# Kernel tuning notes

Hardware: AMD Instinct MI355X
Metric: run time of the kernel (lower is better)

The kernel has to match this reference:

```python
import jax, jax.numpy as jnp
import numpy as np

# --- constants matching DILConfig ---
N_DIFF = 1000      # num_diffusion_steps
STEPS = 4          # inference_steps
S_MAX = 4          # max_scales
BUDGET = 0.2       # entropy_budget
G0 = 2.0           # guidance_strength
ENT_LO = 0.1       # stability_threshold_low
ENT_HI = 0.5       # stability_threshold_high
B, L, C, H = 16, 1024, 128, 512


def setup_inputs() -> dict:
    key = jax.random.key(0)
    ks = jax.random.split(key, 6)
    y_obs = jax.random.normal(ks[0], (B, L, C), dtype=jnp.float32)
    mask = (jax.random.uniform(ks[1], (B, L, C)) > 0.5).astype(jnp.float32)
    z_init = jax.random.normal(ks[2], (B, L, C), dtype=jnp.float32)
    W1 = jax.random.normal(ks[3], (C, H), dtype=jnp.float32) / np.sqrt(C)
    b1 = jnp.zeros((H,), dtype=jnp.float32)
    W2 = jax.random.normal(ks[4], (H, C), dtype=jnp.float32) / np.sqrt(H)
    b2 = jnp.zeros((C,), dtype=jnp.float32)
    tw = jax.random.normal(ks[5], (H,), dtype=jnp.float32)
    return {"y_obs": y_obs, "mask": mask, "z_init": z_init,
            "W1": W1, "b1": b1, "W2": W2, "b2": b2, "tw": tw}


def _dil_forward(y_obs, mask, z_init, W1, b1, W2, b2, tw):
    # diffusion schedule (linear betas)
    betas = jnp.linspace(1e-4, 0.02, N_DIFF, dtype=jnp.float32)
    ac = jnp.cumprod(1.0 - betas)
    alpha = jnp.sqrt(ac)                     # sqrt_alphas_cumprod
    sigma = jnp.sqrt(1.0 - ac)               # sqrt_one_minus_alphas_cumprod
    lam = jnp.log(alpha) - jnp.log(sigma)    # log-SNR/2

    step = N_DIFF // STEPS
    ks = [N_DIFF - 1 - i * step for i in range(STEPS)]

    def score(z, k):
        # epsilon predictor: channel MLP with scalar time feature
        t_feat = jnp.float32(k) / N_DIFF
        h = jax.nn.gelu(jnp.einsum('blc,ch->blh', z, W1) + b1 + t_feat * tw)
        return jnp.einsum('blh,hc->blc', h, W2) + b2

    z = z_init
    for k in ks:  # fixed small unrolled loop over inference steps
        kp = max(k - step, 0)
        eps = score(z, k)                                   # [B,L,C]
        h_lam = lam[kp] - lam[k]
        base_a = alpha[kp] / alpha[k]
        base_b = sigma[kp] * (jnp.exp(h_lam) - 1.0)

        # entropy map: batch-mean |eps| per pixel
        ent_pix = jnp.mean(jnp.abs(eps), axis=0)            # [L,C]

        # self-guidance on observed entries
        obs_err = (z - y_obs) * mask
        guidance = -obs_err / (jnp.var(obs_err) + 1e-8)     # [B,L,C]

        z_new = z
        # coarse -> fine so finer-scale selected nodes overwrite coarser ones
        for s in range(S_MAX - 1, -1, -1):
            w = 2 ** s
            pooled = ent_pix.reshape(L // w, w, C // w, w).mean(axis=(1, 3))
            Knodes = max(1, int(BUDGET * pooled.size))
            _, idx = jax.lax.top_k(pooled.ravel(), Knodes)
            selg = jnp.zeros((pooled.size,), jnp.float32).at[idx].set(1.0)
            selg = selg.reshape(pooled.shape)
            sel = jnp.repeat(jnp.repeat(selg, w, axis=0), w, axis=1)     # [L,C]
            ent_up = jnp.repeat(jnp.repeat(pooled, w, axis=0), w, axis=1)

            # adaptive solver order from entropy stability thresholds
            order = (1.0 + (ent_up > ENT_LO).astype(jnp.float32)
                         + (ent_up > ENT_HI).astype(jnp.float32))
            corr = (1.0 + (order - 1.0) * 0.5 * h_lam
                        + (order - 1.0) * (order - 2.0) / 6.0 * h_lam ** 2)
            gs = G0 * ent_up / (ent_up + 1.0)               # adaptive guidance

            cand = base_a * z - base_b * (corr * eps) + gs * guidance
            z_new = jnp.where(sel[None, :, :] > 0, cand, z_new)
        z = z_new
    return z


def reference(y_obs, mask, z_init, W1, b1, W2, b2, tw):
    return _dil_forward(y_obs, mask, z_init, W1, b1, W2, b2, tw)
```

## Files before the change

kernel.cpp:

```cpp
#include <hip/hip_runtime.h>
#include <math.h>
#include <stdint.h>

#define L_DIM 1024
#define C_DIM 128
#define H_DIM 512
#define B_DIM 16
#define LC (L_DIM * C_DIM)
#define BLC (B_DIM * LC)

typedef __attribute__((ext_vector_type(8))) short short8;
typedef __attribute__((ext_vector_type(4))) float floatx4;

__device__ __forceinline__ unsigned fordbits(unsigned u) {
    return (u & 0x80000000u) ? ~u : (u | 0x80000000u);
}

__device__ __forceinline__ void split3(float x, unsigned& uh, unsigned& um,
                                       unsigned& ul) {
    uh = __float_as_uint(x);
    const float r1 = x - __uint_as_float(uh & 0xffff0000u);
    um = __float_as_uint(r1);
    const float r2 = r1 - __uint_as_float(um & 0xffff0000u);
    ul = __float_as_uint(r2);
}

__device__ __forceinline__ float gelu_fast(float x) {
    const float g = 0.7978845608028654f * (x + 0.044715f * x * x * x);
    const float e = __expf(2.0f * g);
    const float t = 1.0f - 2.0f / (e + 1.0f);
    return 0.5f * x * (1.0f + t);
}

__global__ __launch_bounds__(256) void wsplit_kernel(
    const float* __restrict__ W1, const float* __restrict__ W2,
    unsigned short* __restrict__ W1h, unsigned short* __restrict__ W1m,
    unsigned short* __restrict__ W1l, unsigned short* __restrict__ W2h,
    unsigned short* __restrict__ W2m, unsigned short* __restrict__ W2l) {
    const int t = blockIdx.x * 256 + threadIdx.x;
    unsigned uh, um, ul;
    if (t < 65536) {
        const int j = t & 7, lane = (t >> 3) & 63, nt = (t >> 9) & 31,
                  kt = (t >> 14) & 3;
        const int k = kt * 32 + (lane >> 4) * 8 + j;
        const int n = nt * 16 + (lane & 15);
        split3(W1[k * 512 + n], uh, um, ul);
        W1h[t] = (unsigned short)(uh >> 16);
        W1m[t] = (unsigned short)(um >> 16);
        W1l[t] = (unsigned short)(ul >> 16);
    } else {
        const int t2 = t - 65536;
        const int j = t2 & 7, lane = (t2 >> 3) & 63, nt = (t2 >> 9) & 7,
                  kt = (t2 >> 12) & 15;
        const int k = kt * 32 + (lane >> 4) * 8 + j;
        const int n = nt * 16 + (lane & 15);
        split3(W2[k * 128 + n], uh, um, ul);
        W2h[t2] = (unsigned short)(uh >> 16);
        W2m[t2] = (unsigned short)(um >> 16);
        W2l[t2] = (unsigned short)(ul >> 16);
    }
}

#define MFMA6(AH, AM, AL, BH, BM, BL, ACC)                                    \
    ACC = __builtin_amdgcn_mfma_f32_16x16x32_bf16(AL, BH, ACC, 0, 0, 0);      \
    ACC = __builtin_amdgcn_mfma_f32_16x16x32_bf16(AM, BM, ACC, 0, 0, 0);      \
    ACC = __builtin_amdgcn_mfma_f32_16x16x32_bf16(AH, BL, ACC, 0, 0, 0);      \
    ACC = __builtin_amdgcn_mfma_f32_16x16x32_bf16(AM, BH, ACC, 0, 0, 0);      \
    ACC = __builtin_amdgcn_mfma_f32_16x16x32_bf16(AH, BM, ACC, 0, 0, 0);      \
    ACC = __builtin_amdgcn_mfma_f32_16x16x32_bf16(AH, BH, ACC, 0, 0, 0);

__device__ __forceinline__ int swz(int row, int col) {
    return row * 128 + ((((col >> 3) ^ (row & 15))) << 3) + (col & 7);
}

template <int UPD>
__global__ __launch_bounds__(512, 4) void mlp_kernel(
    float* __restrict__ z, const float* __restrict__ y,
    const float* __restrict__ mk,
    const unsigned short* __restrict__ W1h, const unsigned short* __restrict__ W1m,
    const unsigned short* __restrict__ W1l, const unsigned short* __restrict__ W2h,
    const unsigned short* __restrict__ W2m, const unsigned short* __restrict__ W2l,
    const float* __restrict__ b1, const float* __restrict__ tw,
    const float* __restrict__ b2, float t_feat,
    float* __restrict__ eps_buf, float* __restrict__ ent,
    const float* __restrict__ cA, const float* __restrict__ cB,
    const float* __restrict__ cG, float* __restrict__ accum) {
    __shared__ unsigned short zA[3][4096];
    __shared__ unsigned short hA[3][4096];
    __shared__ float red1[8], red2[8];
    const int tid = threadIdx.x;
    const int w = tid >> 6, lane = tid & 63;
    const int quad = lane >> 4, m16 = lane & 15;
    const int l0 = blockIdx.x * 2;

    float s1 = 0.f, s2 = 0.f;
#pragma unroll
    for (int e = 0; e < 2; ++e) {
        const int f = tid * 8 + e * 4;
        const int r_ = f >> 7, cb = f & 127;
        const int b = r_ & 15, il = r_ >> 4, l = l0 + il;
        const size_t g = ((size_t)b * 1024 + l) * 128 + cb;
        float4 zv = *(const float4*)(z + g);
        const float4 yv = *(const float4*)(y + g);
        const float4 mv = *(const float4*)(mk + g);
        if (UPD) {
            const float4 ev = *(const float4*)(eps_buf + g);
            const int pix = l * 128 + cb;
            const float4 a4 = *(const float4*)(cA + pix);
            const float4 b4 = *(const float4*)(cB + pix);
            const float4 g4 = *(const float4*)(cG + pix);
            zv.x = a4.x * zv.x - b4.x * ev.x - g4.x * ((zv.x - yv.x) * mv.x);
            zv.y = a4.y * zv.y - b4.y * ev.y - g4.y * ((zv.y - yv.y) * mv.y);
            zv.z = a4.z * zv.z - b4.z * ev.z - g4.z * ((zv.z - yv.z) * mv.z);
            zv.w = a4.w * zv.w - b4.w * ev.w - g4.w * ((zv.w - yv.w) * mv.w);
            *(float4*)(z + g) = zv;
        }
        float oe;
        oe = (zv.x - yv.x) * mv.x; s1 += oe; s2 += oe * oe;
        oe = (zv.y - yv.y) * mv.y; s1 += oe; s2 += oe * oe;
        oe = (zv.z - yv.z) * mv.z; s1 += oe; s2 += oe * oe;
        oe = (zv.w - yv.w) * mv.w; s1 += oe; s2 += oe * oe;

        const int base = swz(r_, cb);
        const float xs[4] = {zv.x, zv.y, zv.z, zv.w};
        ushort4 vh, vm, vl;
        unsigned uh, um, ul;
        split3(xs[0], uh, um, ul); vh.x = uh >> 16; vm.x = um >> 16; vl.x = ul >> 16;
        split3(xs[1], uh, um, ul); vh.y = uh >> 16; vm.y = um >> 16; vl.y = ul >> 16;
        split3(xs[2], uh, um, ul); vh.z = uh >> 16; vm.z = um >> 16; vl.z = ul >> 16;
        split3(xs[3], uh, um, ul); vh.w = uh >> 16; vm.w = um >> 16; vl.w = ul >> 16;
        *(ushort4*)(&zA[0][base]) = vh;
        *(ushort4*)(&zA[1][base]) = vm;
        *(ushort4*)(&zA[2][base]) = vl;
    }
#pragma unroll
    for (int off = 32; off; off >>= 1) {
        s1 += __shfl_down(s1, off);
        s2 += __shfl_down(s2, off);
    }
    if (lane == 0) { red1[w] = s1; red2[w] = s2; }
    __syncthreads();
    if (tid == 0) {
        float a1 = 0.f, a2 = 0.f;
#pragma unroll
        for (int i = 0; i < 8; ++i) { a1 += red1[i]; a2 += red2[i]; }
        atomicAdd(&accum[0], a1);
        atomicAdd(&accum[1], a2);
    }

    floatx4 acc1[8];
#pragma unroll
    for (int i = 0; i < 8; ++i) acc1[i] = (floatx4){0.f, 0.f, 0.f, 0.f};

#pragma unroll
    for (int kt = 0; kt < 4; ++kt) {
        short8 Ah[2], Am[2], Al[2];
#pragma unroll
        for (int il = 0; il < 2; ++il) {
            const int fb = swz(il * 16 + m16, kt * 32 + quad * 8);
            Ah[il] = *(const short8*)(&zA[0][fb]);
            Am[il] = *(const short8*)(&zA[1][fb]);
            Al[il] = *(const short8*)(&zA[2][fb]);
        }
#pragma unroll
        for (int q = 0; q < 4; ++q) {
            const size_t off = ((size_t)(kt * 32 + q * 8 + w) * 64 + lane) * 8;
            const short8 bh = *(const short8*)(W1h + off);
            const short8 bm = *(const short8*)(W1m + off);
            const short8 bl = *(const short8*)(W1l + off);
#pragma unroll
            for (int il = 0; il < 2; ++il) {
                floatx4 a = acc1[q * 2 + il];
                MFMA6(Ah[il], Am[il], Al[il], bh, bm, bl, a);
                acc1[q * 2 + il] = a;
            }
        }
    }

    floatx4 acc2[2];
    acc2[0] = (floatx4){0.f, 0.f, 0.f, 0.f};
    acc2[1] = (floatx4){0.f, 0.f, 0.f, 0.f};

    for (int q = 0; q < 4; ++q) {
        __syncthreads();
        {
            const int colg = q * 128 + w * 16 + m16;
            const float bb = b1[colg] + t_feat * tw[colg];
            const int kcol = w * 16 + m16;
#pragma unroll
            for (int il = 0; il < 2; ++il) {
#pragma unroll
                for (int r = 0; r < 4; ++r) {
                    const float x = gelu_fast(acc1[q * 2 + il][r] + bb);
                    unsigned uh, um, ul;
                    split3(x, uh, um, ul);
                    const int idx = swz(il * 16 + quad * 4 + r, kcol);
                    hA[0][idx] = (unsigned short)(uh >> 16);
                    hA[1][idx] = (unsigned short)(um >> 16);
                    hA[2][idx] = (unsigned short)(ul >> 16);
                }
            }
        }
        __syncthreads();

#pragma unroll
        for (int ktl = 0; ktl < 4; ++ktl) {
            short8 Ah2[2], Am2[2], Al2[2];
#pragma unroll
            for (int il = 0; il < 2; ++il) {
                const int fb = swz(il * 16 + m16, ktl * 32 + quad * 8);
                Ah2[il] = *(const short8*)(&hA[0][fb]);
                Am2[il] = *(const short8*)(&hA[1][fb]);
                Al2[il] = *(const short8*)(&hA[2][fb]);
            }
            const size_t off =
                ((size_t)((q * 4 + ktl) * 8 + w) * 64 + lane) * 8;
            const short8 bh = *(const short8*)(W2h + off);
            const short8 bm = *(const short8*)(W2m + off);
            const short8 bl = *(const short8*)(W2l + off);
#pragma unroll
            for (int il = 0; il < 2; ++il) {
                floatx4 a = acc2[il];
                MFMA6(Ah2[il], Am2[il], Al2[il], bh, bm, bl, a);
                acc2[il] = a;
            }
        }
    }

    {
        const int col = w * 16 + m16;
        const float bb2 = b2[col];
#pragma unroll
        for (int il = 0; il < 2; ++il) {
            float pa = 0.f;
#pragma unroll
            for (int r = 0; r < 4; ++r) {
                const float e = acc2[il][r] + bb2;
                const int b = quad * 4 + r;
                eps_buf[((size_t)b * 1024 + l0 + il) * 128 + col] = e;
                pa += fabsf(e);
            }
            pa += __shfl_xor(pa, 16);
            pa += __shfl_xor(pa, 32);
            if (quad == 0) ent[(l0 + il) * 128 + col] = pa * (1.0f / 16.0f);
        }
    }
}

__device__ __forceinline__ void gbar(unsigned* c, unsigned target) {
    __syncthreads();
    if (threadIdx.x == 0) {
        atomicAdd(c, 1u);
        while (atomicAdd(c, 0u) < target) __builtin_amdgcn_s_sleep(1);
    }
    __syncthreads();
}

__global__ __launch_bounds__(256, 1) void select_kernel(
    const float* __restrict__ ent, float* __restrict__ p1,
    float* __restrict__ p2, float* __restrict__ p3,
    unsigned* __restrict__ ghist, unsigned* __restrict__ ctr,
    unsigned* __restrict__ gprefix, float* __restrict__ cA,
    float* __restrict__ cB, float* __restrict__ cG,
    const float* __restrict__ accum_si, float base_a, float base_b,
    float h_lam, int si) {
    __shared__ float dataL[2048];
    __shared__ unsigned hist[4][256];
    __shared__ unsigned sh[256];
    __shared__ unsigned sh_dig, sh_krem;
    const int bid = blockIdx.x, t = threadIdx.x;
    const int gid = bid * 256 + t;
    unsigned* cc = &ctr[si];

    int scale, nloc;
    unsigned K;
    if (bid < 64) {
        scale = 0; nloc = 2048; K = 26214u;
        const int base = bid * 2048;
        for (int i = t; i < 2048; i += 256) dataL[i] = ent[base + i];
    } else if (bid < 80) {
        scale = 1; nloc = 2048; K = 6553u;
        const int base = (bid - 64) * 2048;
        for (int i = t; i < 2048; i += 256) {
            const int idx = base + i;
            const int r = idx >> 6, c = idx & 63;
            float s = 0.f;
#pragma unroll
            for (int ii = 0; ii < 2; ++ii)
#pragma unroll
                for (int jj = 0; jj < 2; ++jj)
                    s += ent[((r * 2 + ii) << 7) + c * 2 + jj];
            const float v = s * 0.25f;
            dataL[i] = v;
            atomicExch((unsigned*)&p1[idx], __float_as_uint(v));
        }
    } else if (bid < 84) {
        scale = 2; nloc = 2048; K = 1638u;
        const int base = (bid - 80) * 2048;
        for (int i = t; i < 2048; i += 256) {
            const int idx = base + i;
            const int r = idx >> 5, c = idx & 31;
            float s = 0.f;
#pragma unroll
            for (int ii = 0; ii < 4; ++ii)
#pragma unroll
                for (int jj = 0; jj < 4; ++jj)
                    s += ent[((r * 4 + ii) << 7) + c * 4 + jj];
            const float v = s * 0.0625f;
            dataL[i] = v;
            atomicExch((unsigned*)&p2[idx], __float_as_uint(v));
        }
    } else {
        scale = 3; nloc = 512; K = 409u;
        const int base = (bid - 84) * 512;
        for (int i = t; i < 512; i += 256) {
            const int idx = base + i;
            const int r = idx >> 4, c = idx & 15;
            float s = 0.f;
#pragma unroll
            for (int ii = 0; ii < 8; ++ii)
#pragma unroll
                for (int jj = 0; jj < 8; ++jj)
                    s += ent[((r * 8 + ii) << 7) + c * 8 + jj];
            const float v = s * (1.0f / 64.0f);
            dataL[i] = v;
            atomicExch((unsigned*)&p3[idx], __float_as_uint(v));
        }
    }
    __syncthreads();

    const int wv = t >> 6;
    unsigned prefix = 0u, krem = K;
    for (int p = 0; p < 4; ++p) {
        const int shift = 24 - 8 * p;
        const unsigned hmask = p ? (0xFFFFFFFFu << (shift + 8)) : 0u;
#pragma unroll
        for (int i = t; i < 1024; i += 256) ((unsigned*)hist)[i] = 0u;
        __syncthreads();
        for (int i = t; i < nloc; i += 256) {
            const unsigned u = fordbits(__float_as_uint(dataL[i]));
            if ((u & hmask) == (prefix & hmask))
                atomicAdd(&hist[wv][(u >> shift) & 255u], 1u);
        }
        __syncthreads();
        const unsigned c = hist[0][t] + hist[1][t] + hist[2][t] + hist[3][t];
        unsigned* gh = &ghist[((si * 4 + p) * 4 + scale) * 256];
        if (c) atomicAdd(&gh[t], c);
        gbar(cc, 88u * (unsigned)(p + 1));
        sh[t] = atomicAdd(&gh[t], 0u);
        __syncthreads();
#pragma unroll
        for (int off = 1; off < 256; off <<= 1) {
            const unsigned v = (t + off < 256) ? sh[t + off] : 0u;
            __syncthreads();
            sh[t] += v;
            __syncthreads();
        }
        const unsigned suf = sh[t];
        const unsigned sufn = (t < 255) ? sh[t + 1] : 0u;
        if (suf >= krem && sufn < krem) {
            sh_dig = (unsigned)t;
            sh_krem = krem - sufn;
        }
        __syncthreads();
        prefix |= (sh_dig << shift);
        krem = sh_krem;
        __syncthreads();
    }
    if (t == 0 && (bid == 0 || bid == 64 || bid == 80 || bid == 84))
        atomicExch(&gprefix[scale], prefix);
    gbar(cc, 88u * 5u);

    const unsigned t0 = atomicAdd(&gprefix[0], 0u);
    const unsigned t1 = atomicAdd(&gprefix[1], 0u);
    const unsigned t2 = atomicAdd(&gprefix[2], 0u);
    const unsigned t3 = atomicAdd(&gprefix[3], 0u);
    const float mean = accum_si[0] * (1.0f / (float)BLC);
    const float var = accum_si[1] * (1.0f / (float)BLC) - mean * mean;
    const float vinv = 1.0f / (var + 1e-8f);

    for (int i = gid; i < LC; i += 22528) {
        const int l = i >> 7, c = i & 127;
        float ent_v = 0.f;
        bool sel = false;
        const float v0 = ent[i];
        if (fordbits(__float_as_uint(v0)) >= t0) { ent_v = v0; sel = true; }
        else {
            const float v1 = __uint_as_float(atomicAdd(
                (unsigned*)&p1[((l >> 1) << 6) + (c >> 1)], 0u));
            if (fordbits(__float_as_uint(v1)) >= t1) { ent_v = v1; sel = true; }
            else {
                const float v2 = __uint_as_float(atomicAdd(
                    (unsigned*)&p2[((l >> 2) << 5) + (c >> 2)], 0u));
                if (fordbits(__float_as_uint(v2)) >= t2) { ent_v = v2; sel = true; }
                else {
                    const float v3 = __uint_as_float(atomicAdd(
                        (unsigned*)&p3[((l >> 3) << 4) + (c >> 3)], 0u));
                    if (fordbits(__float_as_uint(v3)) >= t3) { ent_v = v3; sel = true; }
                }
            }
        }
        if (sel) {
            float corr;
            if (ent_v > 0.5f)
                corr = 1.0f + h_lam + h_lam * h_lam * (1.0f / 3.0f);
            else if (ent_v > 0.1f)
                corr = 1.0f + 0.5f * h_lam;
            else
                corr = 1.0f;
            cA[i] = base_a;
            cB[i] = base_b * corr;
            cG[i] = (2.0f * ent_v / (ent_v + 1.0f)) * vinv;
        } else {
            cA[i] = 1.0f;
            cB[i] = 0.f;
            cG[i] = 0.f;
        }
    }
}

__global__ __launch_bounds__(256) void update_kernel(
    float* __restrict__ z, const float* __restrict__ y,
    const float* __restrict__ mk, const float* __restrict__ eps,
    const float* __restrict__ cA, const float* __restrict__ cB,
    const float* __restrict__ cG) {
    const int idx = blockIdx.x * 256 + threadIdx.x;
    const int p = idx & (LC - 1);
    const float zi = z[idx];
    z[idx] = cA[p] * zi - cB[p] * eps[idx] - cG[p] * ((zi - y[idx]) * mk[idx]);
}

extern "C" void kernel_launch(void* const* d_in, const int* in_sizes, int n_in,
                              void* d_out, int out_size, void* d_ws,
                              size_t ws_size, hipStream_t stream) {
    const float* y_obs = (const float*)d_in[0];
    const float* mask = (const float*)d_in[1];
    const float* z_init = (const float*)d_in[2];
    const float* W1 = (const float*)d_in[3];
    const float* b1 = (const float*)d_in[4];
    const float* W2 = (const float*)d_in[5];
    const float* b2 = (const float*)d_in[6];
    const float* tw = (const float*)d_in[7];
    float* z = (float*)d_out;
    float* ws = (float*)d_ws;

    float* eps = ws;
    float* ent = ws + 2097152;
    float* p1 = ws + 2228224;
    float* p2 = ws + 2260992;
    float* p3 = ws + 2269184;
    float* cA = ws + 2271232;
    float* cB = ws + 2402304;
    float* cG = ws + 2533376;
    unsigned* ghist = (unsigned*)(ws + 2664448);
    unsigned* ctr = (unsigned*)(ws + 2680832);
    float* accum = ws + 2680836;
    unsigned* gprefix = (unsigned*)(ws + 2680844);
    unsigned short* W1h = (unsigned short*)(ws + 2680848);
    unsigned short* W1m = (unsigned short*)(ws + 2713616);
    unsigned short* W1l = (unsigned short*)(ws + 2746384);
    unsigned short* W2h = (unsigned short*)(ws + 2779152);
    unsigned short* W2m = (unsigned short*)(ws + 2811920);
    unsigned short* W2l = (unsigned short*)(ws + 2844688);

    float alpha_[1000], sigma_[1000], lam_[1000];
    {
        float ac = 1.0f;
        for (int i = 0; i < 1000; ++i) {
            const float beta = 1e-4f + (0.02f - 1e-4f) * ((float)i / 999.0f);
            ac = ac * (1.0f - beta);
            alpha_[i] = sqrtf(ac);
            sigma_[i] = sqrtf(1.0f - ac);
            lam_[i] = logf(alpha_[i]) - logf(sigma_[i]);
        }
    }
    float tf[4], hl[4], ba[4], bb[4];
    for (int si = 0; si < 4; ++si) {
        const int k = 999 - si * 250;
        const int kp = (k - 250 > 0) ? (k - 250) : 0;
        tf[si] = (float)k / 1000.0f;
        hl[si] = lam_[kp] - lam_[k];
        ba[si] = alpha_[kp] / alpha_[k];
        bb[si] = sigma_[kp] * (expf(hl[si]) - 1.0f);
    }

    hipMemcpyAsync(z, z_init, sizeof(float) * BLC, hipMemcpyDeviceToDevice,
                   stream);
    hipMemsetAsync(ghist, 0, (16384 + 4 + 8 + 4) * sizeof(unsigned), stream);
    wsplit_kernel<<<512, 256, 0, stream>>>(W1, W2, W1h, W1m, W1l, W2h, W2m,
                                           W2l);

    for (int si = 0; si < 4; ++si) {
        if (si == 0) {
            mlp_kernel<0><<<512, 512, 0, stream>>>(
                z, y_obs, mask, W1h, W1m, W1l, W2h, W2m, W2l, b1, tw, b2,
                tf[0], eps, ent, cA, cB, cG, accum);
        } else {
            mlp_kernel<1><<<512, 512, 0, stream>>>(
                z, y_obs, mask, W1h, W1m, W1l, W2h, W2m, W2l, b1, tw, b2,
                tf[si], eps, ent, cA, cB, cG, accum + 2 * si);
        }
        select_kernel<<<88, 256, 0, stream>>>(
            ent, p1, p2, p3, ghist, ctr, gprefix, cA, cB, cG,
            accum + 2 * si, ba[si], bb[si], hl[si], si);
    }
    update_kernel<<<8192, 256, 0, stream>>>(z, y_obs, mask, eps, cA, cB, cG);
}
```

Baseline: 450.0 us.

## Halve rows per MLP block to double grid size and drop z init copy

```diff
diff --git a/kernel.cpp b/kernel.cpp
--- a/kernel.cpp
+++ b/kernel.cpp
@@ -75,8 +75,8 @@
 
 template <int UPD>
 __global__ __launch_bounds__(512, 4) void mlp_kernel(
-    float* __restrict__ z, const float* __restrict__ y,
-    const float* __restrict__ mk,
+    const float* __restrict__ zin, float* __restrict__ z,
+    const float* __restrict__ y, const float* __restrict__ mk,
     const unsigned short* __restrict__ W1h, const unsigned short* __restrict__ W1m,
     const unsigned short* __restrict__ W1l, const unsigned short* __restrict__ W2h,
     const unsigned short* __restrict__ W2m, const unsigned short* __restrict__ W2l,
@@ -85,27 +85,25 @@
     float* __restrict__ eps_buf, float* __restrict__ ent,
     const float* __restrict__ cA, const float* __restrict__ cB,
     const float* __restrict__ cG, float* __restrict__ accum) {
-    __shared__ unsigned short zA[3][4096];
-    __shared__ unsigned short hA[3][4096];
+    __shared__ unsigned short zA[3][2048];
+    __shared__ unsigned short hA[3][2048];
     __shared__ float red1[8], red2[8];
     const int tid = threadIdx.x;
     const int w = tid >> 6, lane = tid & 63;
     const int quad = lane >> 4, m16 = lane & 15;
-    const int l0 = blockIdx.x * 2;
+    const int l0 = blockIdx.x;
 
     float s1 = 0.f, s2 = 0.f;
-#pragma unroll
-    for (int e = 0; e < 2; ++e) {
-        const int f = tid * 8 + e * 4;
+    {
+        const int f = tid * 4;
         const int r_ = f >> 7, cb = f & 127;
-        const int b = r_ & 15, il = r_ >> 4, l = l0 + il;
-        const size_t g = ((size_t)b * 1024 + l) * 128 + cb;
-        float4 zv = *(const float4*)(z + g);
+        const size_t g = ((size_t)r_ * 1024 + l0) * 128 + cb;
+        float4 zv = *(const float4*)(zin + g);
         const float4 yv = *(const float4*)(y + g);
         const float4 mv = *(const float4*)(mk + g);
         if (UPD) {
             const float4 ev = *(const float4*)(eps_buf + g);
-            const int pix = l * 128 + cb;
+            const int pix = l0 * 128 + cb;
             const float4 a4 = *(const float4*)(cA + pix);
             const float4 b4 = *(const float4*)(cB + pix);
             const float4 g4 = *(const float4*)(cG + pix);
@@ -113,8 +111,8 @@
             zv.y = a4.y * zv.y - b4.y * ev.y - g4.y * ((zv.y - yv.y) * mv.y);
             zv.z = a4.z * zv.z - b4.z * ev.z - g4.z * ((zv.z - yv.z) * mv.z);
             zv.w = a4.w * zv.w - b4.w * ev.w - g4.w * ((zv.w - yv.w) * mv.w);
-            *(float4*)(z + g) = zv;
-        }
+        }
+        *(float4*)(z + g) = zv;
         float oe;
         oe = (zv.x - yv.x) * mv.x; s1 += oe; s2 += oe * oe;
         oe = (zv.y - yv.y) * mv.y; s1 += oe; s2 += oe * oe;
@@ -148,38 +146,29 @@
         atomicAdd(&accum[1], a2);
     }
 
-    floatx4 acc1[8];
-#pragma unroll
-    for (int i = 0; i < 8; ++i) acc1[i] = (floatx4){0.f, 0.f, 0.f, 0.f};
+    floatx4 acc1[4];
+#pragma unroll
+    for (int i = 0; i < 4; ++i) acc1[i] = (floatx4){0.f, 0.f, 0.f, 0.f};
 
 #pragma unroll
     for (int kt = 0; kt < 4; ++kt) {
-        short8 Ah[2], Am[2], Al[2];
-#pragma unroll
-        for (int il = 0; il < 2; ++il) {
-            const int fb = swz(il * 16 + m16, kt * 32 + quad * 8);
-            Ah[il] = *(const short8*)(&zA[0][fb]);
-            Am[il] = *(const short8*)(&zA[1][fb]);
-            Al[il] = *(const short8*)(&zA[2][fb]);
-        }
+        const int fb = swz(m16, kt * 32 + quad * 8);
+        const short8 Ah = *(const short8*)(&zA[0][fb]);
+        const short8 Am = *(const short8*)(&zA[1][fb]);
+        const short8 Al = *(const short8*)(&zA[2][fb]);
 #pragma unroll
         for (int q = 0; q < 4; ++q) {
             const size_t off = ((size_t)(kt * 32 + q * 8 + w) * 64 + lane) * 8;
             const short8 bh = *(const short8*)(W1h + off);
             const short8 bm = *(const short8*)(W1m + off);
             const short8 bl = *(const short8*)(W1l + off);
-#pragma unroll
-            for (int il = 0; il < 2; ++il) {
-                floatx4 a = acc1[q * 2 + il];
-                MFMA6(Ah[il], Am[il], Al[il], bh, bm, bl, a);
-                acc1[q * 2 + il] = a;
-            }
-        }
-    }
-
-    floatx4 acc2[2];
-    acc2[0] = (floatx4){0.f, 0.f, 0.f, 0.f};
-    acc2[1] = (floatx4){0.f, 0.f, 0.f, 0.f};
+            floatx4 a = acc1[q];
+            MFMA6(Ah, Am, Al, bh, bm, bl, a);
+            acc1[q] = a;
+        }
+    }
+
+    floatx4 acc2 = (floatx4){0.f, 0.f, 0.f, 0.f};
 
     for (int q = 0; q < 4; ++q) {
         __syncthreads();
@@ -188,62 +177,47 @@
             const float bb = b1[colg] + t_feat * tw[colg];
             const int kcol = w * 16 + m16;
 #pragma unroll
-            for (int il = 0; il < 2; ++il) {
-#pragma unroll
-                for (int r = 0; r < 4; ++r) {
-                    const float x = gelu_fast(acc1[q * 2 + il][r] + bb);
-                    unsigned uh, um, ul;
-                    split3(x, uh, um, ul);
-                    const int idx = swz(il * 16 + quad * 4 + r, kcol);
-                    hA[0][idx] = (unsigned short)(uh >> 16);
-                    hA[1][idx] = (unsigned short)(um >> 16);
-                    hA[2][idx] = (unsigned short)(ul >> 16);
-                }
+            for (int r = 0; r < 4; ++r) {
+                const float x = gelu_fast(acc1[q][r] + bb);
+                unsigned uh, um, ul;
+                split3(x, uh, um, ul);
+                const int idx = swz(quad * 4 + r, kcol);
+                hA[0][idx] = (unsigned short)(uh >> 16);
+                hA[1][idx] = (unsigned short)(um >> 16);
+                hA[2][idx] = (unsigned short)(ul >> 16);
             }
         }
         __syncthreads();
 
 #pragma unroll
         for (int ktl = 0; ktl < 4; ++ktl) {
-            short8 Ah2[2], Am2[2], Al2[2];
-#pragma unroll
-            for (int il = 0; il < 2; ++il) {
-                const int fb = swz(il * 16 + m16, ktl * 32 + quad * 8);
-                Ah2[il] = *(const short8*)(&hA[0][fb]);
-                Am2[il] = *(const short8*)(&hA[1][fb]);
-                Al2[il] = *(const short8*)(&hA[2][fb]);
-            }
+            const int fb = swz(m16, ktl * 32 + quad * 8);
+            const short8 Ah2 = *(const short8*)(&hA[0][fb]);
+            const short8 Am2 = *(const short8*)(&hA[1][fb]);
+            const short8 Al2 = *(const short8*)(&hA[2][fb]);
             const size_t off =
                 ((size_t)((q * 4 + ktl) * 8 + w) * 64 + lane) * 8;
             const short8 bh = *(const short8*)(W2h + off);
             const short8 bm = *(const short8*)(W2m + off);
             const short8 bl = *(const short8*)(W2l + off);
-#pragma unroll
-            for (int il = 0; il < 2; ++il) {
-                floatx4 a = acc2[il];
-                MFMA6(Ah2[il], Am2[il], Al2[il], bh, bm, bl, a);
-                acc2[il] = a;
-            }
+            MFMA6(Ah2, Am2, Al2, bh, bm, bl, acc2);
         }
     }
 
     {
         const int col = w * 16 + m16;
         const float bb2 = b2[col];
-#pragma unroll
-        for (int il = 0; il < 2; ++il) {
-            float pa = 0.f;
-#pragma unroll
-            for (int r = 0; r < 4; ++r) {
-                const float e = acc2[il][r] + bb2;
-                const int b = quad * 4 + r;
-                eps_buf[((size_t)b * 1024 + l0 + il) * 128 + col] = e;
-                pa += fabsf(e);
-            }
-            pa += __shfl_xor(pa, 16);
-            pa += __shfl_xor(pa, 32);
-            if (quad == 0) ent[(l0 + il) * 128 + col] = pa * (1.0f / 16.0f);
-        }
+        float pa = 0.f;
+#pragma unroll
+        for (int r = 0; r < 4; ++r) {
+            const float e = acc2[r] + bb2;
+            const int b = quad * 4 + r;
+            eps_buf[((size_t)b * 1024 + l0) * 128 + col] = e;
+            pa += fabsf(e);
+        }
+        pa += __shfl_xor(pa, 16);
+        pa += __shfl_xor(pa, 32);
+        if (quad == 0) ent[l0 * 128 + col] = pa * (1.0f / 16.0f);
     }
 }
 
@@ -484,20 +458,18 @@
         bb[si] = sigma_[kp] * (expf(hl[si]) - 1.0f);
     }
 
-    hipMemcpyAsync(z, z_init, sizeof(float) * BLC, hipMemcpyDeviceToDevice,
-                   stream);
     hipMemsetAsync(ghist, 0, (16384 + 4 + 8 + 4) * sizeof(unsigned), stream);
     wsplit_kernel<<<512, 256, 0, stream>>>(W1, W2, W1h, W1m, W1l, W2h, W2m,
                                            W2l);
 
     for (int si = 0; si < 4; ++si) {
         if (si == 0) {
-            mlp_kernel<0><<<512, 512, 0, stream>>>(
-                z, y_obs, mask, W1h, W1m, W1l, W2h, W2m, W2l, b1, tw, b2,
-                tf[0], eps, ent, cA, cB, cG, accum);
+            mlp_kernel<0><<<1024, 512, 0, stream>>>(
+                z_init, z, y_obs, mask, W1h, W1m, W1l, W2h, W2m, W2l, b1, tw,
+                b2, tf[0], eps, ent, cA, cB, cG, accum);
         } else {
-            mlp_kernel<1><<<512, 512, 0, stream>>>(
-                z, y_obs, mask, W1h, W1m, W1l, W2h, W2m, W2l, b1, tw, b2,
+            mlp_kernel<1><<<1024, 512, 0, stream>>>(
+                z, z, y_obs, mask, W1h, W1m, W1l, W2h, W2m, W2l, b1, tw, b2,
                 tf[si], eps, ent, cA, cB, cG, accum + 2 * si);
         }
         select_kernel<<<88, 256, 0, stream>>>(
```

Result: slower. 539.3 us (+19.8%).

## Pack hi/mid bf16 splits in LDS, halve acc1 registers, drop z_init memcpy

Applied to the files above, without the earlier changes.

```diff
diff --git a/kernel.cpp b/kernel.cpp
--- a/kernel.cpp
+++ b/kernel.cpp
@@ -69,14 +69,31 @@
     ACC = __builtin_amdgcn_mfma_f32_16x16x32_bf16(AH, BM, ACC, 0, 0, 0);      \
     ACC = __builtin_amdgcn_mfma_f32_16x16x32_bf16(AH, BH, ACC, 0, 0, 0);
 
-__device__ __forceinline__ int swz(int row, int col) {
-    return row * 128 + ((((col >> 3) ^ (row & 15))) << 3) + (col & 7);
+__device__ __forceinline__ void ldsA(const unsigned* hm,
+                                     const unsigned short* lr, int row,
+                                     int kbase, short8& Ah, short8& Am,
+                                     short8& Al) {
+    const unsigned* p = &hm[row * 132 + kbase];
+    const uint4 a = *(const uint4*)p;
+    const uint4 b = *(const uint4*)(p + 4);
+    union { short8 v; unsigned u[4]; } ah, am;
+    ah.u[0] = (a.x & 0xffffu) | (a.y << 16);
+    ah.u[1] = (a.z & 0xffffu) | (a.w << 16);
+    ah.u[2] = (b.x & 0xffffu) | (b.y << 16);
+    ah.u[3] = (b.z & 0xffffu) | (b.w << 16);
+    am.u[0] = (a.x >> 16) | (a.y & 0xffff0000u);
+    am.u[1] = (a.z >> 16) | (a.w & 0xffff0000u);
+    am.u[2] = (b.x >> 16) | (b.y & 0xffff0000u);
+    am.u[3] = (b.z >> 16) | (b.w & 0xffff0000u);
+    Ah = ah.v;
+    Am = am.v;
+    Al = *(const short8*)(&lr[row * 136 + kbase]);
 }
 
 template <int UPD>
-__global__ __launch_bounds__(512, 4) void mlp_kernel(
-    float* __restrict__ z, const float* __restrict__ y,
-    const float* __restrict__ mk,
+__global__ __launch_bounds__(512, 2) void mlp_kernel(
+    const float* __restrict__ zin, float* __restrict__ z,
+    const float* __restrict__ y, const float* __restrict__ mk,
     const unsigned short* __restrict__ W1h, const unsigned short* __restrict__ W1m,
     const unsigned short* __restrict__ W1l, const unsigned short* __restrict__ W2h,
     const unsigned short* __restrict__ W2m, const unsigned short* __restrict__ W2l,
@@ -85,8 +102,10 @@
     float* __restrict__ eps_buf, float* __restrict__ ent,
     const float* __restrict__ cA, const float* __restrict__ cB,
     const float* __restrict__ cG, float* __restrict__ accum) {
-    __shared__ unsigned short zA[3][4096];
-    __shared__ unsigned short hA[3][4096];
+    __shared__ unsigned lds_hm[32 * 132];
+    __shared__ unsigned short lds_l[32 * 136];
+    __shared__ unsigned h_hm[32 * 132];
+    __shared__ unsigned short h_l[32 * 136];
     __shared__ float red1[8], red2[8];
     const int tid = threadIdx.x;
     const int w = tid >> 6, lane = tid & 63;
@@ -100,7 +119,7 @@
         const int r_ = f >> 7, cb = f & 127;
         const int b = r_ & 15, il = r_ >> 4, l = l0 + il;
         const size_t g = ((size_t)b * 1024 + l) * 128 + cb;
-        float4 zv = *(const float4*)(z + g);
+        float4 zv = *(const float4*)(zin + g);
         const float4 yv = *(const float4*)(y + g);
         const float4 mv = *(const float4*)(mk + g);
         if (UPD) {
@@ -113,25 +132,22 @@
             zv.y = a4.y * zv.y - b4.y * ev.y - g4.y * ((zv.y - yv.y) * mv.y);
             zv.z = a4.z * zv.z - b4.z * ev.z - g4.z * ((zv.z - yv.z) * mv.z);
             zv.w = a4.w * zv.w - b4.w * ev.w - g4.w * ((zv.w - yv.w) * mv.w);
-            *(float4*)(z + g) = zv;
-        }
+        }
+        *(float4*)(z + g) = zv;
         float oe;
         oe = (zv.x - yv.x) * mv.x; s1 += oe; s2 += oe * oe;
         oe = (zv.y - yv.y) * mv.y; s1 += oe; s2 += oe * oe;
         oe = (zv.z - yv.z) * mv.z; s1 += oe; s2 += oe * oe;
         oe = (zv.w - yv.w) * mv.w; s1 += oe; s2 += oe * oe;
 
-        const int base = swz(r_, cb);
         const float xs[4] = {zv.x, zv.y, zv.z, zv.w};
-        ushort4 vh, vm, vl;
-        unsigned uh, um, ul;
-        split3(xs[0], uh, um, ul); vh.x = uh >> 16; vm.x = um >> 16; vl.x = ul >> 16;
-        split3(xs[1], uh, um, ul); vh.y = uh >> 16; vm.y = um >> 16; vl.y = ul >> 16;
-        split3(xs[2], uh, um, ul); vh.z = uh >> 16; vm.z = um >> 16; vl.z = ul >> 16;
-        split3(xs[3], uh, um, ul); vh.w = uh >> 16; vm.w = um >> 16; vl.w = ul >> 16;
-        *(ushort4*)(&zA[0][base]) = vh;
-        *(ushort4*)(&zA[1][base]) = vm;
-        *(ushort4*)(&zA[2][base]) = vl;
+#pragma unroll
+        for (int i = 0; i < 4; ++i) {
+            unsigned uh, um, ul;
+            split3(xs[i], uh, um, ul);
+            lds_hm[r_ * 132 + cb + i] = (uh >> 16) | (um & 0xffff0000u);
+            lds_l[r_ * 136 + cb + i] = (unsigned short)(ul >> 16);
+        }
     }
 #pragma unroll
     for (int off = 32; off; off >>= 1) {
@@ -148,81 +164,79 @@
         atomicAdd(&accum[1], a2);
     }
 
-    floatx4 acc1[8];
-#pragma unroll
-    for (int i = 0; i < 8; ++i) acc1[i] = (floatx4){0.f, 0.f, 0.f, 0.f};
-
-#pragma unroll
-    for (int kt = 0; kt < 4; ++kt) {
-        short8 Ah[2], Am[2], Al[2];
-#pragma unroll
-        for (int il = 0; il < 2; ++il) {
-            const int fb = swz(il * 16 + m16, kt * 32 + quad * 8);
-            Ah[il] = *(const short8*)(&zA[0][fb]);
-            Am[il] = *(const short8*)(&zA[1][fb]);
-            Al[il] = *(const short8*)(&zA[2][fb]);
-        }
-#pragma unroll
-        for (int q = 0; q < 4; ++q) {
-            const size_t off = ((size_t)(kt * 32 + q * 8 + w) * 64 + lane) * 8;
-            const short8 bh = *(const short8*)(W1h + off);
-            const short8 bm = *(const short8*)(W1m + off);
-            const short8 bl = *(const short8*)(W1l + off);
-#pragma unroll
-            for (int il = 0; il < 2; ++il) {
-                floatx4 a = acc1[q * 2 + il];
-                MFMA6(Ah[il], Am[il], Al[il], bh, bm, bl, a);
-                acc1[q * 2 + il] = a;
-            }
-        }
-    }
-
     floatx4 acc2[2];
     acc2[0] = (floatx4){0.f, 0.f, 0.f, 0.f};
     acc2[1] = (floatx4){0.f, 0.f, 0.f, 0.f};
 
-    for (int q = 0; q < 4; ++q) {
-        __syncthreads();
-        {
-            const int colg = q * 128 + w * 16 + m16;
-            const float bb = b1[colg] + t_feat * tw[colg];
-            const int kcol = w * 16 + m16;
-#pragma unroll
-            for (int il = 0; il < 2; ++il) {
-#pragma unroll
-                for (int r = 0; r < 4; ++r) {
-                    const float x = gelu_fast(acc1[q * 2 + il][r] + bb);
-                    unsigned uh, um, ul;
-                    split3(x, uh, um, ul);
-                    const int idx = swz(il * 16 + quad * 4 + r, kcol);
-                    hA[0][idx] = (unsigned short)(uh >> 16);
-                    hA[1][idx] = (unsigned short)(um >> 16);
-                    hA[2][idx] = (unsigned short)(ul >> 16);
+    for (int hf = 0; hf < 2; ++hf) {
+        floatx4 acc1[4];
+#pragma unroll
+        for (int i = 0; i < 4; ++i) acc1[i] = (floatx4){0.f, 0.f, 0.f, 0.f};
+
+#pragma unroll
+        for (int kt = 0; kt < 4; ++kt) {
+            short8 Ah[2], Am[2], Al[2];
+#pragma unroll
+            for (int il = 0; il < 2; ++il)
+                ldsA(lds_hm, lds_l, il * 16 + m16, kt * 32 + quad * 8,
+                     Ah[il], Am[il], Al[il]);
+#pragma unroll
+            for (int s = 0; s < 2; ++s) {
+                const int nt1 = (hf * 2 + s) * 8 + w;
+                const size_t off = ((size_t)(kt * 32 + nt1) * 64 + lane) * 8;
+                const short8 bh = *(const short8*)(W1h + off);
+                const short8 bm = *(const short8*)(W1m + off);
+                const short8 bl = *(const short8*)(W1l + off);
+#pragma unroll
+                for (int il = 0; il < 2; ++il) {
+                    floatx4 a = acc1[s * 2 + il];
+                    MFMA6(Ah[il], Am[il], Al[il], bh, bm, bl, a);
+                    acc1[s * 2 + il] = a;
                 }
             }
         }
-        __syncthreads();
-
-#pragma unroll
-        for (int ktl = 0; ktl < 4; ++ktl) {
-            short8 Ah2[2], Am2[2], Al2[2];
-#pragma unroll
-            for (int il = 0; il < 2; ++il) {
-                const int fb = swz(il * 16 + m16, ktl * 32 + quad * 8);
-                Ah2[il] = *(const short8*)(&hA[0][fb]);
-                Am2[il] = *(const short8*)(&hA[1][fb]);
-                Al2[il] = *(const short8*)(&hA[2][fb]);
+
+#pragma unroll
+        for (int s = 0; s < 2; ++s) {
+            const int q = hf * 2 + s;
+            __syncthreads();
+            {
+                const int coll = w * 16 + m16;
+                const int colg = q * 128 + coll;
+                const float bb = b1[colg] + t_feat * tw[colg];
+#pragma unroll
+                for (int il = 0; il < 2; ++il) {
+#pragma unroll
+                    for (int r = 0; r < 4; ++r) {
+                        const float x = gelu_fast(acc1[s * 2 + il][r] + bb);
+                        unsigned uh, um, ul;
+                        split3(x, uh, um, ul);
+                        const int row = il * 16 + quad * 4 + r;
+                        h_hm[row * 132 + coll] = (uh >> 16) | (um & 0xffff0000u);
+                        h_l[row * 136 + coll] = (unsigned short)(ul >> 16);
+                    }
+                }
             }
-            const size_t off =
-                ((size_t)((q * 4 + ktl) * 8 + w) * 64 + lane) * 8;
-            const short8 bh = *(const short8*)(W2h + off);
-            const short8 bm = *(const short8*)(W2m + off);
-            const short8 bl = *(const short8*)(W2l + off);
-#pragma unroll
-            for (int il = 0; il < 2; ++il) {
-                floatx4 a = acc2[il];
-                MFMA6(Ah2[il], Am2[il], Al2[il], bh, bm, bl, a);
-                acc2[il] = a;
+            __syncthreads();
+
+#pragma unroll
+            for (int ktl = 0; ktl < 4; ++ktl) {
+                short8 Ah2[2], Am2[2], Al2[2];
+#pragma unroll
+                for (int il = 0; il < 2; ++il)
+                    ldsA(h_hm, h_l, il * 16 + m16, ktl * 32 + quad * 8,
+                         Ah2[il], Am2[il], Al2[il]);
+                const int ktg = q * 4 + ktl;
+                const size_t off = ((size_t)(ktg * 8 + w) * 64 + lane) * 8;
+                const short8 bh = *(const short8*)(W2h + off);
+                const short8 bm = *(const short8*)(W2m + off);
+                const short8 bl = *(const short8*)(W2l + off);
+#pragma unroll
+                for (int il = 0; il < 2; ++il) {
+                    floatx4 a = acc2[il];
+                    MFMA6(Ah2[il], Am2[il], Al2[il], bh, bm, bl, a);
+                    acc2[il] = a;
+                }
             }
         }
     }
@@ -251,7 +265,7 @@
     __syncthreads();
     if (threadIdx.x == 0) {
         atomicAdd(c, 1u);
-        while (atomicAdd(c, 0u) < target) __builtin_amdgcn_s_sleep(1);
+        while (atomicAdd(c, 0u) < target) __builtin_amdgcn_s_sleep(16);
     }
     __syncthreads();
 }
@@ -484,8 +498,6 @@
         bb[si] = sigma_[kp] * (expf(hl[si]) - 1.0f);
     }
 
-    hipMemcpyAsync(z, z_init, sizeof(float) * BLC, hipMemcpyDeviceToDevice,
-                   stream);
     hipMemsetAsync(ghist, 0, (16384 + 4 + 8 + 4) * sizeof(unsigned), stream);
     wsplit_kernel<<<512, 256, 0, stream>>>(W1, W2, W1h, W1m, W1l, W2h, W2m,
                                            W2l);
@@ -493,11 +505,11 @@
     for (int si = 0; si < 4; ++si) {
         if (si == 0) {
             mlp_kernel<0><<<512, 512, 0, stream>>>(
-                z, y_obs, mask, W1h, W1m, W1l, W2h, W2m, W2l, b1, tw, b2,
-                tf[0], eps, ent, cA, cB, cG, accum);
+                z_init, z, y_obs, mask, W1h, W1m, W1l, W2h, W2m, W2l, b1, tw,
+                b2, tf[0], eps, ent, cA, cB, cG, accum);
         } else {
             mlp_kernel<1><<<512, 512, 0, stream>>>(
-                z, y_obs, mask, W1h, W1m, W1l, W2h, W2m, W2l, b1, tw, b2,
+                z, z, y_obs, mask, W1h, W1m, W1l, W2h, W2m, W2l, b1, tw, b2,
                 tf[si], eps, ent, cA, cB, cG, accum + 2 * si);
         }
         select_kernel<<<88, 256, 0, stream>>>(
```

Result: slower. 466.3 us (+3.6%).

## Split hidden dim into halves, double-buffer weight loads, fold z_init copy into MLP

Applied to the files above, without the earlier changes.

```diff
diff --git a/kernel.cpp b/kernel.cpp
--- a/kernel.cpp
+++ b/kernel.cpp
@@ -75,8 +75,8 @@
 
 template <int UPD>
 __global__ __launch_bounds__(512, 4) void mlp_kernel(
-    float* __restrict__ z, const float* __restrict__ y,
-    const float* __restrict__ mk,
+    const float* __restrict__ zin, float* __restrict__ z,
+    const float* __restrict__ y, const float* __restrict__ mk,
     const unsigned short* __restrict__ W1h, const unsigned short* __restrict__ W1m,
     const unsigned short* __restrict__ W1l, const unsigned short* __restrict__ W2h,
     const unsigned short* __restrict__ W2m, const unsigned short* __restrict__ W2l,
@@ -100,7 +100,7 @@
         const int r_ = f >> 7, cb = f & 127;
         const int b = r_ & 15, il = r_ >> 4, l = l0 + il;
         const size_t g = ((size_t)b * 1024 + l) * 128 + cb;
-        float4 zv = *(const float4*)(z + g);
+        float4 zv = *(const float4*)(zin + g);
         const float4 yv = *(const float4*)(y + g);
         const float4 mv = *(const float4*)(mk + g);
         if (UPD) {
@@ -113,8 +113,8 @@
             zv.y = a4.y * zv.y - b4.y * ev.y - g4.y * ((zv.y - yv.y) * mv.y);
             zv.z = a4.z * zv.z - b4.z * ev.z - g4.z * ((zv.z - yv.z) * mv.z);
             zv.w = a4.w * zv.w - b4.w * ev.w - g4.w * ((zv.w - yv.w) * mv.w);
-            *(float4*)(z + g) = zv;
-        }
+        }
+        *(float4*)(z + g) = zv;
         float oe;
         oe = (zv.x - yv.x) * mv.x; s1 += oe; s2 += oe * oe;
         oe = (zv.y - yv.y) * mv.y; s1 += oe; s2 += oe * oe;
@@ -148,81 +148,114 @@
         atomicAdd(&accum[1], a2);
     }
 
-    floatx4 acc1[8];
-#pragma unroll
-    for (int i = 0; i < 8; ++i) acc1[i] = (floatx4){0.f, 0.f, 0.f, 0.f};
-
-#pragma unroll
-    for (int kt = 0; kt < 4; ++kt) {
-        short8 Ah[2], Am[2], Al[2];
-#pragma unroll
-        for (int il = 0; il < 2; ++il) {
-            const int fb = swz(il * 16 + m16, kt * 32 + quad * 8);
-            Ah[il] = *(const short8*)(&zA[0][fb]);
-            Am[il] = *(const short8*)(&zA[1][fb]);
-            Al[il] = *(const short8*)(&zA[2][fb]);
-        }
-#pragma unroll
-        for (int q = 0; q < 4; ++q) {
-            const size_t off = ((size_t)(kt * 32 + q * 8 + w) * 64 + lane) * 8;
-            const short8 bh = *(const short8*)(W1h + off);
-            const short8 bm = *(const short8*)(W1m + off);
-            const short8 bl = *(const short8*)(W1l + off);
-#pragma unroll
-            for (int il = 0; il < 2; ++il) {
-                floatx4 a = acc1[q * 2 + il];
-                MFMA6(Ah[il], Am[il], Al[il], bh, bm, bl, a);
-                acc1[q * 2 + il] = a;
-            }
-        }
-    }
-
     floatx4 acc2[2];
     acc2[0] = (floatx4){0.f, 0.f, 0.f, 0.f};
     acc2[1] = (floatx4){0.f, 0.f, 0.f, 0.f};
 
-    for (int q = 0; q < 4; ++q) {
-        __syncthreads();
-        {
-            const int colg = q * 128 + w * 16 + m16;
-            const float bb = b1[colg] + t_feat * tw[colg];
-            const int kcol = w * 16 + m16;
+    for (int hf = 0; hf < 2; ++hf) {
+        floatx4 acc1[4];
+#pragma unroll
+        for (int i = 0; i < 4; ++i) acc1[i] = (floatx4){0.f, 0.f, 0.f, 0.f};
+
+        short8 Wb[2][2][3];
+#pragma unroll
+        for (int s = 0; s < 2; ++s) {
+            const int nt1 = (hf * 2 + s) * 8 + w;
+            const size_t off = ((size_t)nt1 * 64 + lane) * 8;
+            Wb[0][s][0] = *(const short8*)(W1h + off);
+            Wb[0][s][1] = *(const short8*)(W1m + off);
+            Wb[0][s][2] = *(const short8*)(W1l + off);
+        }
+#pragma unroll
+        for (int kt = 0; kt < 4; ++kt) {
+            const int cur = kt & 1;
+            if (kt < 3) {
+#pragma unroll
+                for (int s = 0; s < 2; ++s) {
+                    const int nt1 = (hf * 2 + s) * 8 + w;
+                    const size_t off =
+                        ((size_t)((kt + 1) * 32 + nt1) * 64 + lane) * 8;
+                    Wb[cur ^ 1][s][0] = *(const short8*)(W1h + off);
+                    Wb[cur ^ 1][s][1] = *(const short8*)(W1m + off);
+                    Wb[cur ^ 1][s][2] = *(const short8*)(W1l + off);
+                }
+            }
+            short8 Ah[2], Am[2], Al[2];
 #pragma unroll
             for (int il = 0; il < 2; ++il) {
-#pragma unroll
-                for (int r = 0; r < 4; ++r) {
-                    const float x = gelu_fast(acc1[q * 2 + il][r] + bb);
-                    unsigned uh, um, ul;
-                    split3(x, uh, um, ul);
-                    const int idx = swz(il * 16 + quad * 4 + r, kcol);
-                    hA[0][idx] = (unsigned short)(uh >> 16);
-                    hA[1][idx] = (unsigned short)(um >> 16);
-                    hA[2][idx] = (unsigned short)(ul >> 16);
-                }
-            }
-        }
-        __syncthreads();
-
-#pragma unroll
-        for (int ktl = 0; ktl < 4; ++ktl) {
-            short8 Ah2[2], Am2[2], Al2[2];
-#pragma unroll
-            for (int il = 0; il < 2; ++il) {
-                const int fb = swz(il * 16 + m16, ktl * 32 + quad * 8);
-                Ah2[il] = *(const short8*)(&hA[0][fb]);
-                Am2[il] = *(const short8*)(&hA[1][fb]);
-                Al2[il] = *(const short8*)(&hA[2][fb]);
-            }
-            const size_t off =
-                ((size_t)((q * 4 + ktl) * 8 + w) * 64 + lane) * 8;
-            const short8 bh = *(const short8*)(W2h + off);
-            const short8 bm = *(const short8*)(W2m + off);
-            const short8 bl = *(const short8*)(W2l + off);
-#pragma unroll
-            for (int il = 0; il < 2; ++il) {
-                floatx4 a = acc2[il];
-                MFMA6(Ah2[il], Am2[il], Al2[il], bh, bm, bl, a);
-                acc2[il] = a;
+                const int fb = swz(il * 16 + m16, kt * 32 + quad * 8);
+                Ah[il] = *(const short8*)(&zA[0][fb]);
+                Am[il] = *(const short8*)(&zA[1][fb]);
+                Al[il] = *(const short8*)(&zA[2][fb]);
+            }
+#pragma unroll
+            for (int s = 0; s < 2; ++s) {
+#pragma unroll
+                for (int il = 0; il < 2; ++il) {
+                    floatx4 a = acc1[s * 2 + il];
+                    MFMA6(Ah[il], Am[il], Al[il], Wb[cur][s][0], Wb[cur][s][1],
+                          Wb[cur][s][2], a);
+                    acc1[s * 2 + il] = a;
+                }
+            }
+        }
+
+#pragma unroll
+        for (int s = 0; s < 2; ++s) {
+            const int q = hf * 2 + s;
+            short8 W2b[2][3];
+            {
+                const size_t off0 = ((size_t)((q * 4) * 8 + w) * 64 + lane) * 8;
+                W2b[0][0] = *(const short8*)(W2h + off0);
+                W2b[0][1] = *(const short8*)(W2m + off0);
+                W2b[0][2] = *(const short8*)(W2l + off0);
+            }
+            __syncthreads();
+            {
+                const int kcol = w * 16 + m16;
+                const int colg = q * 128 + kcol;
+                const float bb = b1[colg] + t_feat * tw[colg];
+#pragma unroll
+                for (int il = 0; il < 2; ++il) {
+#pragma unroll
+                    for (int r = 0; r < 4; ++r) {
+                        const float x = gelu_fast(acc1[s * 2 + il][r] + bb);
+                        unsigned uh, um, ul;
+                        split3(x, uh, um, ul);
+                        const int idx = swz(il * 16 + quad * 4 + r, kcol);
+                        hA[0][idx] = (unsigned short)(uh >> 16);
+                        hA[1][idx] = (unsigned short)(um >> 16);
+                        hA[2][idx] = (unsigned short)(ul >> 16);
+                    }
+                }
+            }
+            __syncthreads();
+
+#pragma unroll
+            for (int ktl = 0; ktl < 4; ++ktl) {
+                const int cur = ktl & 1;
+                if (ktl < 3) {
+                    const size_t offn =
+                        ((size_t)((q * 4 + ktl + 1) * 8 + w) * 64 + lane) * 8;
+                    W2b[cur ^ 1][0] = *(const short8*)(W2h + offn);
+                    W2b[cur ^ 1][1] = *(const short8*)(W2m + offn);
+                    W2b[cur ^ 1][2] = *(const short8*)(W2l + offn);
+                }
+                short8 Ah2[2], Am2[2], Al2[2];
+#pragma unroll
+                for (int il = 0; il < 2; ++il) {
+                    const int fb = swz(il * 16 + m16, ktl * 32 + quad * 8);
+                    Ah2[il] = *(const short8*)(&hA[0][fb]);
+                    Am2[il] = *(const short8*)(&hA[1][fb]);
+                    Al2[il] = *(const short8*)(&hA[2][fb]);
+                }
+#pragma unroll
+                for (int il = 0; il < 2; ++il) {
+                    floatx4 a = acc2[il];
+                    MFMA6(Ah2[il], Am2[il], Al2[il], W2b[cur][0], W2b[cur][1],
+                          W2b[cur][2], a);
+                    acc2[il] = a;
+                }
             }
         }
     }
@@ -251,7 +284,7 @@
     __syncthreads();
     if (threadIdx.x == 0) {
         atomicAdd(c, 1u);
-        while (atomicAdd(c, 0u) < target) __builtin_amdgcn_s_sleep(1);
+        while (atomicAdd(c, 0u) < target) __builtin_amdgcn_s_sleep(16);
     }
     __syncthreads();
 }
@@ -484,8 +517,6 @@
         bb[si] = sigma_[kp] * (expf(hl[si]) - 1.0f);
     }
 
-    hipMemcpyAsync(z, z_init, sizeof(float) * BLC, hipMemcpyDeviceToDevice,
-                   stream);
     hipMemsetAsync(ghist, 0, (16384 + 4 + 8 + 4) * sizeof(unsigned), stream);
     wsplit_kernel<<<512, 256, 0, stream>>>(W1, W2, W1h, W1m, W1l, W2h, W2m,
                                            W2l);
@@ -493,11 +524,11 @@
     for (int si = 0; si < 4; ++si) {
         if (si == 0) {
             mlp_kernel<0><<<512, 512, 0, stream>>>(
-                z, y_obs, mask, W1h, W1m, W1l, W2h, W2m, W2l, b1, tw, b2,
-                tf[0], eps, ent, cA, cB, cG, accum);
+                z_init, z, y_obs, mask, W1h, W1m, W1l, W2h, W2m, W2l, b1, tw,
+                b2, tf[0], eps, ent, cA, cB, cG, accum);
         } else {
             mlp_kernel<1><<<512, 512, 0, stream>>>(
-                z, y_obs, mask, W1h, W1m, W1l, W2h, W2m, W2l, b1, tw, b2,
+                z, z, y_obs, mask, W1h, W1m, W1l, W2h, W2m, W2l, b1, tw, b2,
                 tf[si], eps, ent, cA, cB, cG, accum + 2 * si);
         }
         select_kernel<<<88, 256, 0, stream>>>(
```

Result: faster. 433.9 us (-3.6%).
